# Optimization experiments

Measured on AMD Instinct MI355X. Metric: run time of the kernel, lower is better.

The kernel has to match this reference:

```python
import jax, jax.numpy as jnp
import numpy as np

WINDOW = 5
PAD = 2  # (window_size - 1) // 2 for dilation=1


def _layernorm(x, gamma, beta, eps=1e-5):
    # fp32 LayerNorm over last dim, cast back to input dtype
    orig = x.dtype
    x32 = x.astype(jnp.float32)
    mu = jnp.mean(x32, axis=-1, keepdims=True)
    var = jnp.var(x32, axis=-1, keepdims=True)
    y = (x32 - mu) * jax.lax.rsqrt(var + eps) * gamma + beta
    return y.astype(orig)


def _forward(x, ln_gamma, ln_beta, T):
    L, N, D = x.shape  # L = 1 + P tokens, N = B*T
    P = L - 1
    B = N // T
    xn = _layernorm(x, ln_gamma, ln_beta)

    # UnfoldTemporalWindows: x[1:] -> (N, D, P) -> (B, T, D, P), window over T
    patches = jnp.transpose(xn[1:], (1, 2, 0))            # (N, D, P)
    xv = patches.reshape(B, T, D, P)
    xp = jnp.pad(xv, ((0, 0), (PAD, PAD), (0, 0), (0, 0)))
    idx = jnp.arange(T)[:, None] + jnp.arange(WINDOW)[None, :]  # (T, W)
    win = xp[:, idx]                                       # (B, T, W, D, P)
    win = jnp.transpose(win, (0, 1, 3, 2, 4)).reshape(N, D, WINDOW * P)
    upfold = jnp.transpose(win, (2, 0, 1))                 # (O, N, D), O = W*P

    # Correlation_Module: sigmoid affinity of CLS token vs windowed tokens
    cls = xn[:1]                                           # (1, N, D)
    aff = jnp.einsum('lnd,ond->lon', cls, upfold) / jnp.sqrt(jnp.asarray(D, cls.dtype))
    feat = jnp.einsum('lon,ond->lnd', jax.nn.sigmoid(aff) - 0.5, upfold)
    return feat  # (1, N, D)


def setup_inputs() -> dict:
    key = jax.random.key(0)
    k1, = jax.random.split(key, 1)
    L, N, D = 197, 128, 768
    x = jax.random.normal(k1, (L, N, D), dtype=jnp.float32)
    ln_gamma = jnp.ones((D,), dtype=jnp.float32)
    ln_beta = jnp.zeros((D,), dtype=jnp.float32)
    return {"x": x, "ln_gamma": ln_gamma, "ln_beta": ln_beta, "T": 16}


def reference(x, ln_gamma, ln_beta, T):
    return _forward(x, ln_gamma, ln_beta, T)
```

## Files before the change

kernel.cpp:

```cpp
#include <hip/hip_runtime.h>

#define NN 128
#define DD 768
#define TT 16
#define PP 196
#define SCL 0.03608439182435161f
#define VS 776

typedef short short8 __attribute__((ext_vector_type(8)));
typedef short short4v __attribute__((ext_vector_type(4)));
typedef float f32x4 __attribute__((ext_vector_type(4)));

static __device__ __forceinline__ ushort f2bf(float f) {
    union { float f; unsigned int u; } a; a.f = f;
    unsigned int r = a.u + 0x7fffu + ((a.u >> 16) & 1u);
    return (ushort)(r >> 16);
}
static __device__ __forceinline__ float bf2f(ushort u) {
    union { unsigned int u; float f; } c; c.u = (unsigned int)u << 16; return c.f;
}

__global__ __launch_bounds__(256) void k_lnq(const float* __restrict__ x,
                                             const float* __restrict__ gamma,
                                             const float* __restrict__ beta,
                                             ushort* __restrict__ qn) {
    int row  = (blockIdx.x << 2) + (threadIdx.x >> 6);
    int lane = threadIdx.x & 63;
    const float4* xr = (const float4*)(x + (size_t)row * DD);
    float4 v[3];
    float s = 0.f, ss = 0.f;
#pragma unroll
    for (int j = 0; j < 3; ++j) {
        v[j] = xr[lane + 64 * j];
        s  += v[j].x + v[j].y + v[j].z + v[j].w;
        ss = fmaf(v[j].x, v[j].x, ss); ss = fmaf(v[j].y, v[j].y, ss);
        ss = fmaf(v[j].z, v[j].z, ss); ss = fmaf(v[j].w, v[j].w, ss);
    }
#pragma unroll
    for (int o = 32; o > 0; o >>= 1) { s += __shfl_xor(s, o); ss += __shfl_xor(ss, o); }
    float mu  = s * (1.f / DD);
    float var = fmaf(ss, 1.f / DD, -mu * mu);
    float rs  = rsqrtf(var + 1e-5f);
    const float4* g4 = (const float4*)gamma;
    const float4* b4 = (const float4*)beta;
    ushort4* outr = (ushort4*)(qn + (size_t)row * DD);
#pragma unroll
    for (int j = 0; j < 3; ++j) {
        int i4 = lane + 64 * j;
        float4 g = g4[i4], b = b4[i4];
        ushort4 o4;
        o4.x = f2bf((v[j].x - mu) * rs * g.x + b.x);
        o4.y = f2bf((v[j].y - mu) * rs * g.y + b.y);
        o4.z = f2bf((v[j].z - mu) * rs * g.z + b.z);
        o4.w = f2bf((v[j].w - mu) * rs * g.w + b.w);
        outr[i4] = o4;
    }
}

__global__ __launch_bounds__(256) void k_zero(float* __restrict__ out) {
    out[blockIdx.x * 256 + threadIdx.x] = 0.f;
}

template<bool USE_PART>
__global__ __launch_bounds__(256, 4) void k_attn(const float* __restrict__ x,
                                                 const float* __restrict__ gamma,
                                                 const float* __restrict__ beta,
                                                 const ushort* __restrict__ qn,
                                                 ushort* __restrict__ part,
                                                 float* __restrict__ out) {
    __shared__ ushort Vl[16 * VS];
    __shared__ float  Sl[4][TT][17];
    __shared__ ushort Wl[TT][TT];

    int gid = blockIdx.x;
    int b = gid & 7, p = gid >> 3;
    int w = threadIdx.x >> 6, l = threadIdx.x & 63;
    int l15 = l & 15, lh = l >> 4;

    int r   = w * 4 + lh;
    int j16 = l15;
    const float* vrow = x + ((size_t)(1 + p) * NN + b * TT + r) * DD;
    float4 c[12];
#pragma unroll
    for (int k = 0; k < 12; ++k) c[k] = *(const float4*)(vrow + (j16 + 16 * k) * 4);

    const ushort* qrow = qn + (size_t)(b * TT + l15) * DD + w * 192 + lh * 8;
    short8 qf[6];
#pragma unroll
    for (int s = 0; s < 6; ++s) qf[s] = *(const short8*)(qrow + s * 32);

    float s1 = 0.f, s2 = 0.f;
#pragma unroll
    for (int k = 0; k < 12; ++k) {
        float4 v = c[k];
        s1 += v.x + v.y + v.z + v.w;
        s2 = fmaf(v.x, v.x, s2); s2 = fmaf(v.y, v.y, s2);
        s2 = fmaf(v.z, v.z, s2); s2 = fmaf(v.w, v.w, s2);
    }
#pragma unroll
    for (int o = 1; o < 16; o <<= 1) { s1 += __shfl_xor(s1, o); s2 += __shfl_xor(s2, o); }
    float mu  = s1 * (1.f / DD);
    float var = fmaf(s2, 1.f / DD, -mu * mu);
    float rs  = rsqrtf(var + 1e-5f);

    const float4* g4 = (const float4*)gamma;
    const float4* b4 = (const float4*)beta;
#pragma unroll
    for (int k = 0; k < 12; ++k) {
        int c4 = j16 + 16 * k;
        float4 g = g4[c4], e = b4[c4];
        float4 v = c[k];
        ushort4 ut;
        ut.x = f2bf((v.x - mu) * rs * g.x + e.x);
        ut.y = f2bf((v.y - mu) * rs * g.y + e.y);
        ut.z = f2bf((v.z - mu) * rs * g.z + e.z);
        ut.w = f2bf((v.w - mu) * rs * g.w + e.w);
        *(ushort4*)&Vl[r * VS + c4 * 4] = ut;
    }
    __syncthreads();

    f32x4 sacc = (f32x4){0.f, 0.f, 0.f, 0.f};
#pragma unroll
    for (int s = 0; s < 6; ++s) {
        int k0 = w * 192 + s * 32 + lh * 8;
        short8 bfr = *(const short8*)&Vl[l15 * VS + k0];
        sacc = __builtin_amdgcn_mfma_f32_16x16x32_bf16(qf[s], bfr, sacc, 0, 0, 0);
    }
#pragma unroll
    for (int q = 0; q < 4; ++q) Sl[w][lh * 4 + q][l15] = sacc[q];
    __syncthreads();

    {
        int t  = threadIdx.x >> 4, rr = threadIdx.x & 15;
        float s = Sl[0][t][rr] + Sl[1][t][rr] + Sl[2][t][rr] + Sl[3][t][rr];
        int dlt = rr - t;
        float wv = (dlt <= 2 && dlt >= -2)
                     ? (1.f / (1.f + __expf(-s * SCL)) - 0.5f) : 0.f;
        Wl[t][rr] = f2bf(wv);
    }
    __syncthreads();

    short8 wfrag = (short8){0, 0, 0, 0, 0, 0, 0, 0};
    if (lh < 2) wfrag = *(const short8*)&Wl[l15][lh * 8];
    ushort* myp = part + ((size_t)(p * 8 + b)) * (TT * DD);
#pragma unroll
    for (int i = 0; i < 12; ++i) {
        int d0 = w * 192 + i * 16;
        union { ushort sv[8]; short8 v; } u;
        u.v = (short8){0, 0, 0, 0, 0, 0, 0, 0};
        if (lh < 2) {
#pragma unroll
            for (int j = 0; j < 8; ++j)
                u.sv[j] = Vl[(lh * 8 + j) * VS + d0 + l15];
        }
        f32x4 a = __builtin_amdgcn_mfma_f32_16x16x32_bf16(
            wfrag, u.v, (f32x4){0.f, 0.f, 0.f, 0.f}, 0, 0, 0);
        if (USE_PART) {
            ushort4 pk;
            pk.x = f2bf(a[0]); pk.y = f2bf(a[1]);
            pk.z = f2bf(a[2]); pk.w = f2bf(a[3]);
            *(ushort4*)&myp[((w * 12 + i) * 64 + l) * 4] = pk;
        } else {
#pragma unroll
            for (int q = 0; q < 4; ++q)
                atomicAdd(out + (size_t)(b * TT + lh * 4 + q) * DD + d0 + l15, a[q]);
        }
    }
}

__global__ __launch_bounds__(256) void k_reduce(const ushort* __restrict__ part,
                                                float* __restrict__ out) {
    int bid = blockIdx.x;
    int pc  = bid % 7;
    int g   = (bid / 7) * 256 + threadIdx.x;
    int b    = g / 3072;
    int pos4 = g - b * 3072;
    const ushort* src = part + (size_t)b * (TT * DD) + pos4 * 4;

    float s0 = 0.f, s1 = 0.f, s2 = 0.f, s3 = 0.f;
#pragma unroll 4
    for (int p = pc * 28; p < pc * 28 + 28; ++p) {
        union { short4v v; ushort sv[4]; } u;
        u.v = *(const short4v*)(src + (size_t)p * 8 * (TT * DD));
        s0 += bf2f(u.sv[0]); s1 += bf2f(u.sv[1]);
        s2 += bf2f(u.sv[2]); s3 += bf2f(u.sv[3]);
    }
    int fp    = pos4 * 4;
    int chunk = fp >> 8;
    int l     = (fp >> 2) & 63;
    int w     = chunk / 12, i = chunk - w * 12;
    int lh    = l >> 4,   l15 = l & 15;
    int d     = w * 192 + i * 16 + l15;
    float* dst = out + ((size_t)b * TT + lh * 4) * DD + d;
    atomicAdd(dst,            s0);
    atomicAdd(dst + 1 * DD,   s1);
    atomicAdd(dst + 2 * DD,   s2);
    atomicAdd(dst + 3 * DD,   s3);
}

extern "C" void kernel_launch(void* const* d_in, const int* in_sizes, int n_in,
                              void* d_out, int out_size, void* d_ws, size_t ws_size,
                              hipStream_t stream) {
    const float* x     = (const float*)d_in[0];
    const float* gamma = (const float*)d_in[1];
    const float* beta  = (const float*)d_in[2];
    float* out = (float*)d_out;

    const size_t qn_bytes   = (size_t)NN * DD * 2;
    const size_t part_bytes = (size_t)PP * 8 * TT * DD * 2;
    ushort* qn   = (ushort*)d_ws;
    ushort* part = (ushort*)((char*)d_ws + qn_bytes);
    bool use_part = ws_size >= qn_bytes + part_bytes;

    k_zero<<<NN * DD / 256, 256, 0, stream>>>(out);
    k_lnq<<<NN / 4, 256, 0, stream>>>(x, gamma, beta, qn);
    if (use_part) {
        k_attn<true><<<8 * PP, 256, 0, stream>>>(x, gamma, beta, qn, part, out);
        k_reduce<<<7 * 96, 256, 0, stream>>>(part, out);
    } else {
        k_attn<false><<<8 * PP, 256, 0, stream>>>(x, gamma, beta, qn, part, out);
    }
}
```

Baseline: 43.35 us.

## Process two patches per attention block with prefetch and fold zeroing into LN kernel

Each k_attn block now handles two patch positions, accumulating the second matmul in registers and prefetching the second patch's activations while the first patch's matmuls run. This halves the partial-sum buffer and the reduce kernel's loop trip count, and the output zeroing is merged into k_lnq to drop one kernel launch. The cost is higher register pressure, with launch bounds relaxed from 4 to 3 waves per SIMD, and half as many blocks.

```diff
diff --git a/kernel.cpp b/kernel.cpp
--- a/kernel.cpp
+++ b/kernel.cpp
@@ -4,6 +4,7 @@
 #define DD 768
 #define TT 16
 #define PP 196
+#define NSL 98
 #define SCL 0.03608439182435161f
 #define VS 776
 
@@ -23,7 +24,14 @@
 __global__ __launch_bounds__(256) void k_lnq(const float* __restrict__ x,
                                              const float* __restrict__ gamma,
                                              const float* __restrict__ beta,
-                                             ushort* __restrict__ qn) {
+                                             ushort* __restrict__ qn,
+                                             float* __restrict__ out) {
+    int zi = blockIdx.x * 256 + threadIdx.x;
+    float4 z = {0.f, 0.f, 0.f, 0.f};
+    ((float4*)out)[zi]         = z;
+    ((float4*)out)[zi + 8192]  = z;
+    ((float4*)out)[zi + 16384] = z;
+
     int row  = (blockIdx.x << 2) + (threadIdx.x >> 6);
     int lane = threadIdx.x & 63;
     const float4* xr = (const float4*)(x + (size_t)row * DD);
@@ -57,12 +65,8 @@
     }
 }
 
-__global__ __launch_bounds__(256) void k_zero(float* __restrict__ out) {
-    out[blockIdx.x * 256 + threadIdx.x] = 0.f;
-}
-
 template<bool USE_PART>
-__global__ __launch_bounds__(256, 4) void k_attn(const float* __restrict__ x,
+__global__ __launch_bounds__(256, 3) void k_attn(const float* __restrict__ x,
                                                  const float* __restrict__ gamma,
                                                  const float* __restrict__ beta,
                                                  const ushort* __restrict__ qn,
@@ -73,97 +77,136 @@
     __shared__ ushort Wl[TT][TT];
 
     int gid = blockIdx.x;
-    int b = gid & 7, p = gid >> 3;
+    int b = gid & 7, sl = gid >> 3;
     int w = threadIdx.x >> 6, l = threadIdx.x & 63;
     int l15 = l & 15, lh = l >> 4;
-
-    int r   = w * 4 + lh;
-    int j16 = l15;
-    const float* vrow = x + ((size_t)(1 + p) * NN + b * TT + r) * DD;
-    float4 c[12];
-#pragma unroll
-    for (int k = 0; k < 12; ++k) c[k] = *(const float4*)(vrow + (j16 + 16 * k) * 4);
+    int r = w * 4 + lh, j16 = l15;
 
     const ushort* qrow = qn + (size_t)(b * TT + l15) * DD + w * 192 + lh * 8;
     short8 qf[6];
 #pragma unroll
     for (int s = 0; s < 6; ++s) qf[s] = *(const short8*)(qrow + s * 32);
 
-    float s1 = 0.f, s2 = 0.f;
-#pragma unroll
-    for (int k = 0; k < 12; ++k) {
-        float4 v = c[k];
-        s1 += v.x + v.y + v.z + v.w;
-        s2 = fmaf(v.x, v.x, s2); s2 = fmaf(v.y, v.y, s2);
-        s2 = fmaf(v.z, v.z, s2); s2 = fmaf(v.w, v.w, s2);
-    }
-#pragma unroll
-    for (int o = 1; o < 16; o <<= 1) { s1 += __shfl_xor(s1, o); s2 += __shfl_xor(s2, o); }
-    float mu  = s1 * (1.f / DD);
-    float var = fmaf(s2, 1.f / DD, -mu * mu);
-    float rs  = rsqrtf(var + 1e-5f);
+    f32x4 acc[12];
+#pragma unroll
+    for (int i = 0; i < 12; ++i) acc[i] = (f32x4){0.f, 0.f, 0.f, 0.f};
 
     const float4* g4 = (const float4*)gamma;
     const float4* b4 = (const float4*)beta;
-#pragma unroll
-    for (int k = 0; k < 12; ++k) {
-        int c4 = j16 + 16 * k;
-        float4 g = g4[c4], e = b4[c4];
-        float4 v = c[k];
-        ushort4 ut;
-        ut.x = f2bf((v.x - mu) * rs * g.x + e.x);
-        ut.y = f2bf((v.y - mu) * rs * g.y + e.y);
-        ut.z = f2bf((v.z - mu) * rs * g.z + e.z);
-        ut.w = f2bf((v.w - mu) * rs * g.w + e.w);
-        *(ushort4*)&Vl[r * VS + c4 * 4] = ut;
-    }
+    float4 c[12];
+
+#define GLOADP(P)                                                                 \
+    {                                                                             \
+        const float* vrow = x + ((size_t)(1 + (P)) * NN + b * TT + r) * DD;       \
+        _Pragma("unroll")                                                         \
+        for (int k = 0; k < 12; ++k) c[k] = *(const float4*)(vrow + (j16 + 16 * k) * 4); \
+    }
+
+#define LNPACK()                                                                  \
+    {                                                                             \
+        float s1 = 0.f, s2 = 0.f;                                                 \
+        _Pragma("unroll")                                                         \
+        for (int k = 0; k < 12; ++k) {                                            \
+            float4 v = c[k];                                                      \
+            s1 += v.x + v.y + v.z + v.w;                                          \
+            s2 = fmaf(v.x, v.x, s2); s2 = fmaf(v.y, v.y, s2);                     \
+            s2 = fmaf(v.z, v.z, s2); s2 = fmaf(v.w, v.w, s2);                     \
+        }                                                                         \
+        _Pragma("unroll")                                                         \
+        for (int o = 1; o < 16; o <<= 1) {                                        \
+            s1 += __shfl_xor(s1, o); s2 += __shfl_xor(s2, o);                     \
+        }                                                                         \
+        float mu  = s1 * (1.f / DD);                                              \
+        float var = fmaf(s2, 1.f / DD, -mu * mu);                                 \
+        float rs  = rsqrtf(var + 1e-5f);                                          \
+        _Pragma("unroll")                                                         \
+        for (int k = 0; k < 12; ++k) {                                            \
+            int c4 = j16 + 16 * k;                                                \
+            float4 g = g4[c4], e = b4[c4];                                        \
+            float4 v = c[k];                                                      \
+            ushort4 ut;                                                           \
+            ut.x = f2bf((v.x - mu) * rs * g.x + e.x);                             \
+            ut.y = f2bf((v.y - mu) * rs * g.y + e.y);                             \
+            ut.z = f2bf((v.z - mu) * rs * g.z + e.z);                             \
+            ut.w = f2bf((v.w - mu) * rs * g.w + e.w);                             \
+            *(ushort4*)&Vl[r * VS + c4 * 4] = ut;                                 \
+        }                                                                         \
+    }
+
+#define MM1W()                                                                    \
+    {                                                                             \
+        f32x4 sacc = (f32x4){0.f, 0.f, 0.f, 0.f};                                 \
+        _Pragma("unroll")                                                         \
+        for (int s = 0; s < 6; ++s) {                                             \
+            int k0 = w * 192 + s * 32 + lh * 8;                                   \
+            short8 bfr = *(const short8*)&Vl[l15 * VS + k0];                      \
+            sacc = __builtin_amdgcn_mfma_f32_16x16x32_bf16(qf[s], bfr, sacc, 0, 0, 0); \
+        }                                                                         \
+        _Pragma("unroll")                                                         \
+        for (int q = 0; q < 4; ++q) Sl[w][lh * 4 + q][l15] = sacc[q];             \
+        __syncthreads();                                                          \
+        {                                                                         \
+            int t  = threadIdx.x >> 4, rr = threadIdx.x & 15;                     \
+            float s = Sl[0][t][rr] + Sl[1][t][rr] + Sl[2][t][rr] + Sl[3][t][rr];  \
+            int dlt = rr - t;                                                     \
+            float wv = (dlt <= 2 && dlt >= -2)                                    \
+                         ? (1.f / (1.f + __expf(-s * SCL)) - 0.5f) : 0.f;         \
+            Wl[t][rr] = f2bf(wv);                                                 \
+        }                                                                         \
+        __syncthreads();                                                          \
+    }
+
+#define MM2()                                                                     \
+    {                                                                             \
+        short8 wfrag = (short8){0, 0, 0, 0, 0, 0, 0, 0};                          \
+        if (lh < 2) wfrag = *(const short8*)&Wl[l15][lh * 8];                     \
+        _Pragma("unroll")                                                         \
+        for (int i = 0; i < 12; ++i) {                                            \
+            int d0 = w * 192 + i * 16;                                            \
+            union { ushort sv[8]; short8 v; } u;                                  \
+            u.v = (short8){0, 0, 0, 0, 0, 0, 0, 0};                               \
+            if (lh < 2) {                                                         \
+                _Pragma("unroll")                                                 \
+                for (int j = 0; j < 8; ++j)                                       \
+                    u.sv[j] = Vl[(lh * 8 + j) * VS + d0 + l15];                   \
+            }                                                                     \
+            acc[i] = __builtin_amdgcn_mfma_f32_16x16x32_bf16(wfrag, u.v, acc[i], 0, 0, 0); \
+        }                                                                         \
+    }
+
+    GLOADP(sl * 2);
+    LNPACK();
     __syncthreads();
-
-    f32x4 sacc = (f32x4){0.f, 0.f, 0.f, 0.f};
-#pragma unroll
-    for (int s = 0; s < 6; ++s) {
-        int k0 = w * 192 + s * 32 + lh * 8;
-        short8 bfr = *(const short8*)&Vl[l15 * VS + k0];
-        sacc = __builtin_amdgcn_mfma_f32_16x16x32_bf16(qf[s], bfr, sacc, 0, 0, 0);
-    }
-#pragma unroll
-    for (int q = 0; q < 4; ++q) Sl[w][lh * 4 + q][l15] = sacc[q];
+    GLOADP(sl * 2 + 1);
+    MM1W();
+    MM2();
     __syncthreads();
-
-    {
-        int t  = threadIdx.x >> 4, rr = threadIdx.x & 15;
-        float s = Sl[0][t][rr] + Sl[1][t][rr] + Sl[2][t][rr] + Sl[3][t][rr];
-        int dlt = rr - t;
-        float wv = (dlt <= 2 && dlt >= -2)
-                     ? (1.f / (1.f + __expf(-s * SCL)) - 0.5f) : 0.f;
-        Wl[t][rr] = f2bf(wv);
-    }
+    LNPACK();
     __syncthreads();
-
-    short8 wfrag = (short8){0, 0, 0, 0, 0, 0, 0, 0};
-    if (lh < 2) wfrag = *(const short8*)&Wl[l15][lh * 8];
-    ushort* myp = part + ((size_t)(p * 8 + b)) * (TT * DD);
-#pragma unroll
-    for (int i = 0; i < 12; ++i) {
-        int d0 = w * 192 + i * 16;
-        union { ushort sv[8]; short8 v; } u;
-        u.v = (short8){0, 0, 0, 0, 0, 0, 0, 0};
-        if (lh < 2) {
-#pragma unroll
-            for (int j = 0; j < 8; ++j)
-                u.sv[j] = Vl[(lh * 8 + j) * VS + d0 + l15];
+    MM1W();
+    MM2();
+
+#undef GLOADP
+#undef LNPACK
+#undef MM1W
+#undef MM2
+
+    if (USE_PART) {
+        ushort* myp = part + (size_t)(sl * 8 + b) * (TT * DD);
+#pragma unroll
+        for (int i = 0; i < 12; ++i) {
+            ushort4 pk;
+            pk.x = f2bf(acc[i][0]); pk.y = f2bf(acc[i][1]);
+            pk.z = f2bf(acc[i][2]); pk.w = f2bf(acc[i][3]);
+            *(ushort4*)&myp[((w * 12 + i) * 64 + l) * 4] = pk;
         }
-        f32x4 a = __builtin_amdgcn_mfma_f32_16x16x32_bf16(
-            wfrag, u.v, (f32x4){0.f, 0.f, 0.f, 0.f}, 0, 0, 0);
-        if (USE_PART) {
-            ushort4 pk;
-            pk.x = f2bf(a[0]); pk.y = f2bf(a[1]);
-            pk.z = f2bf(a[2]); pk.w = f2bf(a[3]);
-            *(ushort4*)&myp[((w * 12 + i) * 64 + l) * 4] = pk;
-        } else {
+    } else {
+#pragma unroll
+        for (int i = 0; i < 12; ++i) {
+            int d0 = w * 192 + i * 16;
 #pragma unroll
             for (int q = 0; q < 4; ++q)
-                atomicAdd(out + (size_t)(b * TT + lh * 4 + q) * DD + d0 + l15, a[q]);
+                atomicAdd(out + (size_t)(b * TT + lh * 4 + q) * DD + d0 + l15, acc[i][q]);
         }
     }
 }
@@ -178,10 +221,10 @@
     const ushort* src = part + (size_t)b * (TT * DD) + pos4 * 4;
 
     float s0 = 0.f, s1 = 0.f, s2 = 0.f, s3 = 0.f;
-#pragma unroll 4
-    for (int p = pc * 28; p < pc * 28 + 28; ++p) {
+#pragma unroll 2
+    for (int s = pc * 14; s < pc * 14 + 14; ++s) {
         union { short4v v; ushort sv[4]; } u;
-        u.v = *(const short4v*)(src + (size_t)p * 8 * (TT * DD));
+        u.v = *(const short4v*)(src + (size_t)s * 8 * (TT * DD));
         s0 += bf2f(u.sv[0]); s1 += bf2f(u.sv[1]);
         s2 += bf2f(u.sv[2]); s3 += bf2f(u.sv[3]);
     }
@@ -192,10 +235,10 @@
     int lh    = l >> 4,   l15 = l & 15;
     int d     = w * 192 + i * 16 + l15;
     float* dst = out + ((size_t)b * TT + lh * 4) * DD + d;
-    atomicAdd(dst,            s0);
-    atomicAdd(dst + 1 * DD,   s1);
-    atomicAdd(dst + 2 * DD,   s2);
-    atomicAdd(dst + 3 * DD,   s3);
+    atomicAdd(dst,          s0);
+    atomicAdd(dst + 1 * DD, s1);
+    atomicAdd(dst + 2 * DD, s2);
+    atomicAdd(dst + 3 * DD, s3);
 }
 
 extern "C" void kernel_launch(void* const* d_in, const int* in_sizes, int n_in,
@@ -207,17 +250,16 @@
     float* out = (float*)d_out;
 
     const size_t qn_bytes   = (size_t)NN * DD * 2;
-    const size_t part_bytes = (size_t)PP * 8 * TT * DD * 2;
+    const size_t part_bytes = (size_t)NSL * 8 * TT * DD * 2;
     ushort* qn   = (ushort*)d_ws;
     ushort* part = (ushort*)((char*)d_ws + qn_bytes);
     bool use_part = ws_size >= qn_bytes + part_bytes;
 
-    k_zero<<<NN * DD / 256, 256, 0, stream>>>(out);
-    k_lnq<<<NN / 4, 256, 0, stream>>>(x, gamma, beta, qn);
+    k_lnq<<<NN / 4, 256, 0, stream>>>(x, gamma, beta, qn, out);
     if (use_part) {
-        k_attn<true><<<8 * PP, 256, 0, stream>>>(x, gamma, beta, qn, part, out);
+        k_attn<true><<<8 * NSL, 256, 0, stream>>>(x, gamma, beta, qn, part, out);
         k_reduce<<<7 * 96, 256, 0, stream>>>(part, out);
     } else {
-        k_attn<false><<<8 * PP, 256, 0, stream>>>(x, gamma, beta, qn, part, out);
-    }
-}
+        k_attn<false><<<8 * NSL, 256, 0, stream>>>(x, gamma, beta, qn, part, out);
+    }
+}
```

Result: faster. 41.39 us (-4.5%).

## Process two patches per block, swizzle LDS, fuse zeroing into LN kernel

Applied to the files above, without the earlier changes.

Each attention block now handles two patch positions (32 value rows) with 512 threads. This halves the block count and the bf16 partial buffer that the reduce kernel reads. The 32 rows are stacked so one MFMA with a full K=32 covers both patches, which removes the zero-padded half of the weight fragment. LDS uses an XOR swizzle instead of padding, the separate zero kernel is folded into the LN kernel, and barriers become explicit lgkmcnt waits. In exchange the block uses more LDS and threads, which may reduce occupancy.

```diff
diff --git a/kernel.cpp b/kernel.cpp
--- a/kernel.cpp
+++ b/kernel.cpp
@@ -4,8 +4,8 @@
 #define DD 768
 #define TT 16
 #define PP 196
+#define NSL 98
 #define SCL 0.03608439182435161f
-#define VS 776
 
 typedef short short8 __attribute__((ext_vector_type(8)));
 typedef short short4v __attribute__((ext_vector_type(4)));
@@ -20,10 +20,27 @@
     union { unsigned int u; float f; } c; c.u = (unsigned int)u << 16; return c.f;
 }
 
+static __device__ __forceinline__ int vidx(int r, int d) {
+    return r * DD + ((((d >> 3) ^ (r & 7)) << 3) | (d & 7));
+}
+
+static __device__ __forceinline__ void bar_lgkm() {
+    asm volatile("s_waitcnt lgkmcnt(0)" ::: "memory");
+    __builtin_amdgcn_s_barrier();
+    __builtin_amdgcn_sched_barrier(0);
+}
+
 __global__ __launch_bounds__(256) void k_lnq(const float* __restrict__ x,
                                              const float* __restrict__ gamma,
                                              const float* __restrict__ beta,
-                                             ushort* __restrict__ qn) {
+                                             ushort* __restrict__ qn,
+                                             float* __restrict__ out) {
+    int zi = blockIdx.x * 256 + threadIdx.x;
+    float4 z = {0.f, 0.f, 0.f, 0.f};
+    ((float4*)out)[zi]         = z;
+    ((float4*)out)[zi + 8192]  = z;
+    ((float4*)out)[zi + 16384] = z;
+
     int row  = (blockIdx.x << 2) + (threadIdx.x >> 6);
     int lane = threadIdx.x & 63;
     const float4* xr = (const float4*)(x + (size_t)row * DD);
@@ -57,113 +74,124 @@
     }
 }
 
-__global__ __launch_bounds__(256) void k_zero(float* __restrict__ out) {
-    out[blockIdx.x * 256 + threadIdx.x] = 0.f;
-}
-
 template<bool USE_PART>
-__global__ __launch_bounds__(256, 4) void k_attn(const float* __restrict__ x,
+__global__ __launch_bounds__(512, 4) void k_attn(const float* __restrict__ x,
                                                  const float* __restrict__ gamma,
                                                  const float* __restrict__ beta,
                                                  const ushort* __restrict__ qn,
                                                  ushort* __restrict__ part,
                                                  float* __restrict__ out) {
-    __shared__ ushort Vl[16 * VS];
-    __shared__ float  Sl[4][TT][17];
-    __shared__ ushort Wl[TT][TT];
+    __shared__ ushort Vl[32 * DD];
+    __shared__ float  Sl[8][TT][33];
+    __shared__ ushort Wl[TT][32];
 
     int gid = blockIdx.x;
-    int b = gid & 7, p = gid >> 3;
+    int b = gid & 7, sl = gid >> 3;
     int w = threadIdx.x >> 6, l = threadIdx.x & 63;
     int l15 = l & 15, lh = l >> 4;
 
-    int r   = w * 4 + lh;
-    int j16 = l15;
-    const float* vrow = x + ((size_t)(1 + p) * NN + b * TT + r) * DD;
-    float4 c[12];
-#pragma unroll
-    for (int k = 0; k < 12; ++k) c[k] = *(const float4*)(vrow + (j16 + 16 * k) * 4);
-
-    const ushort* qrow = qn + (size_t)(b * TT + l15) * DD + w * 192 + lh * 8;
-    short8 qf[6];
-#pragma unroll
-    for (int s = 0; s < 6; ++s) qf[s] = *(const short8*)(qrow + s * 32);
-
-    float s1 = 0.f, s2 = 0.f;
-#pragma unroll
-    for (int k = 0; k < 12; ++k) {
-        float4 v = c[k];
-        s1 += v.x + v.y + v.z + v.w;
-        s2 = fmaf(v.x, v.x, s2); s2 = fmaf(v.y, v.y, s2);
-        s2 = fmaf(v.z, v.z, s2); s2 = fmaf(v.w, v.w, s2);
-    }
-#pragma unroll
-    for (int o = 1; o < 16; o <<= 1) { s1 += __shfl_xor(s1, o); s2 += __shfl_xor(s2, o); }
-    float mu  = s1 * (1.f / DD);
-    float var = fmaf(s2, 1.f / DD, -mu * mu);
-    float rs  = rsqrtf(var + 1e-5f);
-
-    const float4* g4 = (const float4*)gamma;
-    const float4* b4 = (const float4*)beta;
-#pragma unroll
-    for (int k = 0; k < 12; ++k) {
-        int c4 = j16 + 16 * k;
-        float4 g = g4[c4], e = b4[c4];
-        float4 v = c[k];
-        ushort4 ut;
-        ut.x = f2bf((v.x - mu) * rs * g.x + e.x);
-        ut.y = f2bf((v.y - mu) * rs * g.y + e.y);
-        ut.z = f2bf((v.z - mu) * rs * g.z + e.z);
-        ut.w = f2bf((v.w - mu) * rs * g.w + e.w);
-        *(ushort4*)&Vl[r * VS + c4 * 4] = ut;
-    }
-    __syncthreads();
-
-    f32x4 sacc = (f32x4){0.f, 0.f, 0.f, 0.f};
-#pragma unroll
-    for (int s = 0; s < 6; ++s) {
-        int k0 = w * 192 + s * 32 + lh * 8;
-        short8 bfr = *(const short8*)&Vl[l15 * VS + k0];
-        sacc = __builtin_amdgcn_mfma_f32_16x16x32_bf16(qf[s], bfr, sacc, 0, 0, 0);
-    }
-#pragma unroll
-    for (int q = 0; q < 4; ++q) Sl[w][lh * 4 + q][l15] = sacc[q];
-    __syncthreads();
-
-    {
-        int t  = threadIdx.x >> 4, rr = threadIdx.x & 15;
-        float s = Sl[0][t][rr] + Sl[1][t][rr] + Sl[2][t][rr] + Sl[3][t][rr];
-        int dlt = rr - t;
+    {
+        int r = threadIdx.x >> 4, j = threadIdx.x & 15;
+        const float* vrow =
+            x + ((size_t)(1 + sl * 2 + (r >> 4)) * NN + b * TT + (r & 15)) * DD;
+        float4 c[12];
+#pragma unroll
+        for (int k = 0; k < 12; ++k) c[k] = *(const float4*)(vrow + (j + 16 * k) * 4);
+        float s1 = 0.f, s2 = 0.f;
+#pragma unroll
+        for (int k = 0; k < 12; ++k) {
+            float4 v = c[k];
+            s1 += v.x + v.y + v.z + v.w;
+            s2 = fmaf(v.x, v.x, s2); s2 = fmaf(v.y, v.y, s2);
+            s2 = fmaf(v.z, v.z, s2); s2 = fmaf(v.w, v.w, s2);
+        }
+#pragma unroll
+        for (int o = 1; o < 16; o <<= 1) { s1 += __shfl_xor(s1, o); s2 += __shfl_xor(s2, o); }
+        float mu  = s1 * (1.f / DD);
+        float var = fmaf(s2, 1.f / DD, -mu * mu);
+        float rs  = rsqrtf(var + 1e-5f);
+        const float4* g4 = (const float4*)gamma;
+        const float4* b4 = (const float4*)beta;
+#pragma unroll
+        for (int k = 0; k < 12; ++k) {
+            int c4 = j + 16 * k;
+            float4 g = g4[c4], e = b4[c4];
+            float4 v = c[k];
+            ushort4 ut;
+            ut.x = f2bf((v.x - mu) * rs * g.x + e.x);
+            ut.y = f2bf((v.y - mu) * rs * g.y + e.y);
+            ut.z = f2bf((v.z - mu) * rs * g.z + e.z);
+            ut.w = f2bf((v.w - mu) * rs * g.w + e.w);
+            *(ushort4*)&Vl[vidx(r, c4 * 4)] = ut;
+        }
+    }
+    bar_lgkm();
+
+    {
+        const ushort* qrow = qn + (size_t)(b * TT + l15) * DD + w * 96 + lh * 8;
+        short8 qf[3];
+#pragma unroll
+        for (int s = 0; s < 3; ++s) qf[s] = *(const short8*)(qrow + s * 32);
+#pragma unroll
+        for (int cg = 0; cg < 2; ++cg) {
+            f32x4 sacc = (f32x4){0.f, 0.f, 0.f, 0.f};
+            int vr = cg * 16 + l15;
+#pragma unroll
+            for (int s = 0; s < 3; ++s) {
+                int k0 = w * 96 + s * 32 + lh * 8;
+                short8 bfr = *(const short8*)&Vl[vidx(vr, k0)];
+                sacc = __builtin_amdgcn_mfma_f32_16x16x32_bf16(qf[s], bfr, sacc, 0, 0, 0);
+            }
+#pragma unroll
+            for (int q = 0; q < 4; ++q) Sl[w][lh * 4 + q][cg * 16 + l15] = sacc[q];
+        }
+    }
+    bar_lgkm();
+
+    {
+        int t  = threadIdx.x >> 5, rr = threadIdx.x & 31;
+        float s = 0.f;
+#pragma unroll
+        for (int k = 0; k < 8; ++k) s += Sl[k][t][rr];
+        int m = rr & 15;
+        int dlt = m - t;
         float wv = (dlt <= 2 && dlt >= -2)
                      ? (1.f / (1.f + __expf(-s * SCL)) - 0.5f) : 0.f;
         Wl[t][rr] = f2bf(wv);
     }
-    __syncthreads();
-
-    short8 wfrag = (short8){0, 0, 0, 0, 0, 0, 0, 0};
-    if (lh < 2) wfrag = *(const short8*)&Wl[l15][lh * 8];
-    ushort* myp = part + ((size_t)(p * 8 + b)) * (TT * DD);
-#pragma unroll
-    for (int i = 0; i < 12; ++i) {
-        int d0 = w * 192 + i * 16;
-        union { ushort sv[8]; short8 v; } u;
-        u.v = (short8){0, 0, 0, 0, 0, 0, 0, 0};
-        if (lh < 2) {
+    bar_lgkm();
+
+    f32x4 acc[6];
+    {
+        short8 wfrag = *(const short8*)&Wl[l15][lh * 8];
+#pragma unroll
+        for (int i = 0; i < 6; ++i) {
+            int d0 = w * 96 + i * 16;
+            union { ushort sv[8]; short8 v; } u;
 #pragma unroll
             for (int j = 0; j < 8; ++j)
-                u.sv[j] = Vl[(lh * 8 + j) * VS + d0 + l15];
-        }
-        f32x4 a = __builtin_amdgcn_mfma_f32_16x16x32_bf16(
-            wfrag, u.v, (f32x4){0.f, 0.f, 0.f, 0.f}, 0, 0, 0);
-        if (USE_PART) {
+                u.sv[j] = Vl[vidx(lh * 8 + j, d0 + l15)];
+            acc[i] = __builtin_amdgcn_mfma_f32_16x16x32_bf16(
+                wfrag, u.v, (f32x4){0.f, 0.f, 0.f, 0.f}, 0, 0, 0);
+        }
+    }
+
+    if (USE_PART) {
+        ushort* myp = part + (size_t)(sl * 8 + b) * (TT * DD);
+#pragma unroll
+        for (int i = 0; i < 6; ++i) {
             ushort4 pk;
-            pk.x = f2bf(a[0]); pk.y = f2bf(a[1]);
-            pk.z = f2bf(a[2]); pk.w = f2bf(a[3]);
-            *(ushort4*)&myp[((w * 12 + i) * 64 + l) * 4] = pk;
-        } else {
+            pk.x = f2bf(acc[i][0]); pk.y = f2bf(acc[i][1]);
+            pk.z = f2bf(acc[i][2]); pk.w = f2bf(acc[i][3]);
+            *(ushort4*)&myp[((w * 6 + i) * 64 + l) * 4] = pk;
+        }
+    } else {
+#pragma unroll
+        for (int i = 0; i < 6; ++i) {
+            int d0 = w * 96 + i * 16;
 #pragma unroll
             for (int q = 0; q < 4; ++q)
-                atomicAdd(out + (size_t)(b * TT + lh * 4 + q) * DD + d0 + l15, a[q]);
+                atomicAdd(out + (size_t)(b * TT + lh * 4 + q) * DD + d0 + l15, acc[i][q]);
         }
     }
 }
@@ -178,24 +206,24 @@
     const ushort* src = part + (size_t)b * (TT * DD) + pos4 * 4;
 
     float s0 = 0.f, s1 = 0.f, s2 = 0.f, s3 = 0.f;
-#pragma unroll 4
-    for (int p = pc * 28; p < pc * 28 + 28; ++p) {
+#pragma unroll 2
+    for (int s = pc * 14; s < pc * 14 + 14; ++s) {
         union { short4v v; ushort sv[4]; } u;
-        u.v = *(const short4v*)(src + (size_t)p * 8 * (TT * DD));
+        u.v = *(const short4v*)(src + (size_t)s * 8 * (TT * DD));
         s0 += bf2f(u.sv[0]); s1 += bf2f(u.sv[1]);
         s2 += bf2f(u.sv[2]); s3 += bf2f(u.sv[3]);
     }
     int fp    = pos4 * 4;
     int chunk = fp >> 8;
     int l     = (fp >> 2) & 63;
-    int w     = chunk / 12, i = chunk - w * 12;
+    int w     = chunk / 6, i = chunk - w * 6;
     int lh    = l >> 4,   l15 = l & 15;
-    int d     = w * 192 + i * 16 + l15;
+    int d     = w * 96 + i * 16 + l15;
     float* dst = out + ((size_t)b * TT + lh * 4) * DD + d;
-    atomicAdd(dst,            s0);
-    atomicAdd(dst + 1 * DD,   s1);
-    atomicAdd(dst + 2 * DD,   s2);
-    atomicAdd(dst + 3 * DD,   s3);
+    atomicAdd(dst,          s0);
+    atomicAdd(dst + 1 * DD, s1);
+    atomicAdd(dst + 2 * DD, s2);
+    atomicAdd(dst + 3 * DD, s3);
 }
 
 extern "C" void kernel_launch(void* const* d_in, const int* in_sizes, int n_in,
@@ -207,17 +235,16 @@
     float* out = (float*)d_out;
 
     const size_t qn_bytes   = (size_t)NN * DD * 2;
-    const size_t part_bytes = (size_t)PP * 8 * TT * DD * 2;
+    const size_t part_bytes = (size_t)NSL * 8 * TT * DD * 2;
     ushort* qn   = (ushort*)d_ws;
     ushort* part = (ushort*)((char*)d_ws + qn_bytes);
     bool use_part = ws_size >= qn_bytes + part_bytes;
 
-    k_zero<<<NN * DD / 256, 256, 0, stream>>>(out);
-    k_lnq<<<NN / 4, 256, 0, stream>>>(x, gamma, beta, qn);
+    k_lnq<<<NN / 4, 256, 0, stream>>>(x, gamma, beta, qn, out);
     if (use_part) {
-        k_attn<true><<<8 * PP, 256, 0, stream>>>(x, gamma, beta, qn, part, out);
+        k_attn<true><<<8 * NSL, 512, 0, stream>>>(x, gamma, beta, qn, part, out);
         k_reduce<<<7 * 96, 256, 0, stream>>>(part, out);
     } else {
-        k_attn<false><<<8 * PP, 256, 0, stream>>>(x, gamma, beta, qn, part, out);
-    }
-}
+        k_attn<false><<<8 * NSL, 512, 0, stream>>>(x, gamma, beta, qn, part, out);
+    }
+}
```

Measured after the change: 38.67 us, median of 2. 10.8% less time.
